# Kernel optimization log

Hardware: AMD Instinct MI355X
Metric: run time of the kernel (lower is better)

Reference implementation:

```python
import jax, jax.numpy as jnp
import numpy as np
import math

B, S, D, H = 2, 2048, 1024, 16
DH = D // H
FF = 4096
EPS = 1e-5


def _xavier(k, shape):
    lim = math.sqrt(6.0 / (shape[0] + shape[1]))
    return jax.random.uniform(k, shape, jnp.float32, -lim, lim)


def setup_inputs() -> dict:
    key = jax.random.key(0)
    ks = jax.random.split(key, 8)
    return {
        "x": jax.random.normal(ks[0], (B, S, D), jnp.float32),
        "mask": jnp.ones((B, S), jnp.int32),
        "WQ": _xavier(ks[1], (D, D)), "bQ": jnp.zeros((D,), jnp.float32),
        "WK": _xavier(ks[2], (D, D)), "bK": jnp.zeros((D,), jnp.float32),
        "WV": _xavier(ks[3], (D, D)), "bV": jnp.zeros((D,), jnp.float32),
        "WY": _xavier(ks[4], (D, D)), "bY": jnp.zeros((D,), jnp.float32),
        "ln1_w": jnp.ones((D,), jnp.float32), "ln1_b": jnp.zeros((D,), jnp.float32),
        "ln2_w": jnp.ones((D,), jnp.float32), "ln2_b": jnp.zeros((D,), jnp.float32),
        "W1": _xavier(ks[5], (D, FF)), "b1": jnp.zeros((FF,), jnp.float32),
        "W2": _xavier(ks[6], (FF, D)), "b2": jnp.zeros((D,), jnp.float32),
    }


def _layer_norm(x, w, b):
    # manual LayerNorm: biased variance over last dim
    m = jnp.mean(x, axis=-1, keepdims=True)
    v = jnp.mean(jnp.square(x - m), axis=-1, keepdims=True)
    return (x - m) / jnp.sqrt(v + EPS) * w + b


def _attention(x, mask, WQ, bQ, WK, bK, WV, bV, WY, bY):
    b, s, _ = x.shape
    def split(t):  # (B,S,D) -> (B,H,S,DH)
        return t.reshape(b, s, H, DH).transpose(0, 2, 1, 3)
    q = split(x @ WQ + bQ)
    k = split(x @ WK + bK)
    v = split(x @ WV + bV)
    scores = jnp.einsum('bhqd,bhkd->bhqk', q, k) / math.sqrt(DH)
    scores = jnp.where(mask[:, None, None, :] == 0, -jnp.inf, scores)
    w = jax.nn.softmax(scores, axis=-1)
    y = jnp.einsum('bhqk,bhkd->bhqd', w, v)
    y = y.transpose(0, 2, 1, 3).reshape(b, s, D)  # merge heads
    return y @ WY + bY


def reference(x, mask, WQ, bQ, WK, bK, WV, bV, WY, bY,
              ln1_w, ln1_b, ln2_w, ln2_b, W1, b1, W2, b2):
    a = _attention(x, mask, WQ, bQ, WK, bK, WV, bV, WY, bY)
    h = _layer_norm(a + x, ln1_w, ln1_b)
    ff = jax.nn.gelu(h @ W1 + b1, approximate=False) @ W2 + b2
    return _layer_norm(ff + h, ln2_w, ln2_b)
```

## Files before the change

### kernel.cpp

```cpp
#include <hip/hip_runtime.h>
#include <cstdint>
#include <cstddef>

#define B_ 2
#define S_ 2048
#define D_ 1024
#define H_ 16
#define DH_ 64
#define FF_ 4096
#define M_ (B_*S_)
#define MB_ ((size_t)1 << 20)
#define NT_ (S_/64)

using u16 = unsigned short;
using short8 = __attribute__((ext_vector_type(8))) short;
using short4v = __attribute__((ext_vector_type(4))) short;
using floatx4 = __attribute__((ext_vector_type(4))) float;

__device__ __forceinline__ float bf2f(u16 u) {
    return __uint_as_float(((uint32_t)u) << 16);
}
__device__ __forceinline__ u16 f2bf(float f) {
    uint32_t u = __float_as_uint(f);
    u += 0x7fffu + ((u >> 16) & 1u);
    return (u16)(u >> 16);
}
__device__ __forceinline__ uint32_t cvtpk_bf16(float lo, float hi) {
    uint32_t r;
    asm("v_cvt_pk_bf16_f32 %0, %1, %2" : "=v"(r) : "v"(lo), "v"(hi));
    return r;
}
__device__ __forceinline__ void async_copy16(const u16* g, u16* l) {
    __builtin_amdgcn_global_load_lds(
        (const __attribute__((address_space(1))) uint32_t*)g,
        (__attribute__((address_space(3))) uint32_t*)l, 16, 0, 0);
}

__global__ __launch_bounds__(256) void cvt_f32_bf16(
    const float* __restrict__ in, u16* __restrict__ out, int n)
{
    const int i = (blockIdx.x * 256 + threadIdx.x) * 4;
    if (i < n) {
        const float4 v = *(const float4*)(in + i);
        out[i + 0] = f2bf(v.x);
        out[i + 1] = f2bf(v.y);
        out[i + 2] = f2bf(v.z);
        out[i + 3] = f2bf(v.w);
    }
}

__global__ __launch_bounds__(256) void mask_bias(
    const int* __restrict__ mask, float* __restrict__ bias, int n)
{
    const int i = blockIdx.x * 256 + threadIdx.x;
    if (i < n) bias[i] = mask[i] ? 0.f : -1e30f;
}

__global__ void transpose_cvt(const float* __restrict__ in, u16* __restrict__ out,
                              int R, int C) {
    __shared__ float t[32][33];
    const int bx = blockIdx.x * 32, by = blockIdx.y * 32;
    const int tx = threadIdx.x, ty = threadIdx.y;
#pragma unroll
    for (int i = 0; i < 32; i += 8)
        t[ty + i][tx] = in[(size_t)(by + ty + i) * C + bx + tx];
    __syncthreads();
#pragma unroll
    for (int i = 0; i < 32; i += 8)
        out[(size_t)(bx + ty + i) * R + by + tx] = f2bf(t[tx][ty + i]);
}

__global__ void transpose_cvt4(
    const float* __restrict__ WQ, const float* __restrict__ WK,
    const float* __restrict__ WV, const float* __restrict__ WY,
    u16* __restrict__ Wqkvt, u16* __restrict__ WYt)
{
    __shared__ float t[32][33];
    const int zz = blockIdx.z;
    const float* in = zz == 0 ? WQ : zz == 1 ? WK : zz == 2 ? WV : WY;
    u16* out = zz < 3 ? Wqkvt + (size_t)zz * D_ * D_ : WYt;
    const int bx = blockIdx.x * 32, by = blockIdx.y * 32;
    const int tx = threadIdx.x, ty = threadIdx.y;
#pragma unroll
    for (int i = 0; i < 32; i += 8)
        t[ty + i][tx] = in[(size_t)(by + ty + i) * D_ + bx + tx];
    __syncthreads();
#pragma unroll
    for (int i = 0; i < 32; i += 8)
        out[(size_t)(bx + ty + i) * D_ + by + tx] = f2bf(t[tx][ty + i]);
}

template<bool GELU, bool OUT_F32>
__global__ __launch_bounds__(256) void gemm_bt(
    const u16* __restrict__ A, const u16* __restrict__ Bt,
    const float* __restrict__ bias, void* __restrict__ Cout,
    int M, int N, int K)
{
    __shared__ alignas(16) u16 As[128 * 32];
    __shared__ alignas(16) u16 Bs[128 * 32];
    const int tid = threadIdx.x;
    const int w = tid >> 6, lane = tid & 63;
    const int lm = lane & 15, quad = lane >> 4;
    const int wm = w >> 1, wn = w & 1;
    const size_t m0 = (size_t)blockIdx.y * 128, n0 = (size_t)blockIdx.x * 128;

    const int rowS = w * 16 + (lane >> 2);
    const int colS = (lane & 3) * 8;
    const u16* gA = A + (m0 + rowS) * K + colS;
    const u16* gB = Bt + (n0 + rowS) * K + colS;
    u16* lA = As + w * 512;
    u16* lB = Bs + w * 512;

    floatx4 acc[4][4];
    const floatx4 z = {0.f, 0.f, 0.f, 0.f};
#pragma unroll
    for (int i = 0; i < 4; ++i)
#pragma unroll
        for (int j = 0; j < 4; ++j) acc[i][j] = z;

    for (int k0 = 0; k0 < K; k0 += 32) {
        __syncthreads();
        async_copy16(gA, lA);
        async_copy16(gA + (size_t)64 * K, lA + 2048);
        async_copy16(gB, lB);
        async_copy16(gB + (size_t)64 * K, lB + 2048);
        gA += 32; gB += 32;
        __syncthreads();

        short8 af[4], bfr[4];
#pragma unroll
        for (int t = 0; t < 4; ++t)
            af[t] = *(const short8*)&As[(wm * 64 + t * 16 + lm) * 32 + quad * 8];
#pragma unroll
        for (int t = 0; t < 4; ++t)
            bfr[t] = *(const short8*)&Bs[(wn * 64 + t * 16 + lm) * 32 + quad * 8];
#pragma unroll
        for (int i = 0; i < 4; ++i)
#pragma unroll
            for (int j = 0; j < 4; ++j)
                acc[i][j] = __builtin_amdgcn_mfma_f32_16x16x32_bf16(
                    af[i], bfr[j], acc[i][j], 0, 0, 0);
    }

#pragma unroll
    for (int i = 0; i < 4; ++i) {
        const size_t r0 = m0 + wm * 64 + i * 16 + quad * 4;
#pragma unroll
        for (int j = 0; j < 4; ++j) {
            const size_t c = n0 + wn * 64 + j * 16 + lm;
            const float bv = bias[c];
#pragma unroll
            for (int t = 0; t < 4; ++t) {
                float v = acc[i][j][t] + bv;
                if (GELU) v = 0.5f * v * (1.f + erff(v * 0.70710678118f));
                if (OUT_F32) ((float*)Cout)[(r0 + t) * (size_t)N + c] = v;
                else         ((u16*)Cout)[(r0 + t) * (size_t)N + c] = f2bf(v);
            }
        }
    }
}

__global__ __launch_bounds__(256) void gemm_bt_skp(
    const u16* __restrict__ A, const u16* __restrict__ Bt,
    const float* __restrict__ bias, float* __restrict__ out0,
    float* __restrict__ Pext, int M, int N, int K)
{
    __shared__ alignas(16) u16 As[128 * 32];
    __shared__ alignas(16) u16 Bs[128 * 32];
    const int tid = threadIdx.x;
    const int w = tid >> 6, lane = tid & 63;
    const int lm = lane & 15, quad = lane >> 4;
    const int wm = w >> 1, wn = w & 1;
    const int kh = blockIdx.z;
    const int Ks = K / gridDim.z;

    const int nwg = gridDim.x * gridDim.y;
    int bid = blockIdx.y * gridDim.x + blockIdx.x;
    if ((nwg & 7) == 0) {
        const int cpx = nwg >> 3;
        bid = (bid & 7) * cpx + (bid >> 3);
    }
    const int bx = bid % gridDim.x, by = bid / gridDim.x;
    const size_t m0 = (size_t)by * 128, n0 = (size_t)bx * 128;

    const int rowS = w * 16 + (lane >> 2);
    const int colS = (lane & 3) * 8;
    const u16* gA = A + (m0 + rowS) * K + (size_t)kh * Ks + colS;
    const u16* gB = Bt + (n0 + rowS) * K + (size_t)kh * Ks + colS;
    u16* lA = As + w * 512;
    u16* lB = Bs + w * 512;

    floatx4 acc[4][4];
    const floatx4 z = {0.f, 0.f, 0.f, 0.f};
#pragma unroll
    for (int i = 0; i < 4; ++i)
#pragma unroll
        for (int j = 0; j < 4; ++j) acc[i][j] = z;

    for (int k0 = 0; k0 < Ks; k0 += 32) {
        __syncthreads();
        async_copy16(gA, lA);
        async_copy16(gA + (size_t)64 * K, lA + 2048);
        async_copy16(gB, lB);
        async_copy16(gB + (size_t)64 * K, lB + 2048);
        gA += 32; gB += 32;
        __syncthreads();

        short8 af[4], bfr[4];
#pragma unroll
        for (int t = 0; t < 4; ++t)
            af[t] = *(const short8*)&As[(wm * 64 + t * 16 + lm) * 32 + quad * 8];
#pragma unroll
        for (int t = 0; t < 4; ++t)
            bfr[t] = *(const short8*)&Bs[(wn * 64 + t * 16 + lm) * 32 + quad * 8];
#pragma unroll
        for (int i = 0; i < 4; ++i)
#pragma unroll
            for (int j = 0; j < 4; ++j)
                acc[i][j] = __builtin_amdgcn_mfma_f32_16x16x32_bf16(
                    af[i], bfr[j], acc[i][j], 0, 0, 0);
    }

    float* Cout = (kh == 0) ? out0 : Pext + (size_t)(kh - 1) * ((size_t)M * N);
#pragma unroll
    for (int i = 0; i < 4; ++i) {
        const size_t r0 = m0 + wm * 64 + i * 16 + quad * 4;
#pragma unroll
        for (int j = 0; j < 4; ++j) {
            const size_t c = n0 + wn * 64 + j * 16 + lm;
            const float bv = (kh == 0) ? bias[c] : 0.f;
#pragma unroll
            for (int t = 0; t < 4; ++t)
                Cout[(r0 + t) * (size_t)N + c] = acc[i][j][t] + bv;
        }
    }
}

__global__ __launch_bounds__(256) void gemm_bt_sk2(
    const u16* __restrict__ A, const u16* __restrict__ Bt,
    const float* __restrict__ bias, float* __restrict__ Cout,
    int M, int N, int K)
{
    __shared__ alignas(16) u16 As[128 * 32];
    __shared__ alignas(16) u16 Bs[128 * 32];
    const int tid = threadIdx.x;
    const int w = tid >> 6, lane = tid & 63;
    const int lm = lane & 15, quad = lane >> 4;
    const int wm = w >> 1, wn = w & 1;
    const int kh = blockIdx.z;
    const int Ks = K >> 1;
    const size_t m0 = (size_t)blockIdx.y * 128, n0 = (size_t)blockIdx.x * 128;

    const int rowS = w * 16 + (lane >> 2);
    const int colS = (lane & 3) * 8;
    const u16* gA = A + (m0 + rowS) * K + (size_t)kh * Ks + colS;
    const u16* gB = Bt + (n0 + rowS) * K + (size_t)kh * Ks + colS;
    u16* lA = As + w * 512;
    u16* lB = Bs + w * 512;

    floatx4 acc[4][4];
    const floatx4 z = {0.f, 0.f, 0.f, 0.f};
#pragma unroll
    for (int i = 0; i < 4; ++i)
#pragma unroll
        for (int j = 0; j < 4; ++j) acc[i][j] = z;

    for (int k0 = 0; k0 < Ks; k0 += 32) {
        __syncthreads();
        async_copy16(gA, lA);
        async_copy16(gA + (size_t)64 * K, lA + 2048);
        async_copy16(gB, lB);
        async_copy16(gB + (size_t)64 * K, lB + 2048);
        gA += 32; gB += 32;
        __syncthreads();

        short8 af[4], bfr[4];
#pragma unroll
        for (int t = 0; t < 4; ++t)
            af[t] = *(const short8*)&As[(wm * 64 + t * 16 + lm) * 32 + quad * 8];
#pragma unroll
        for (int t = 0; t < 4; ++t)
            bfr[t] = *(const short8*)&Bs[(wn * 64 + t * 16 + lm) * 32 + quad * 8];
#pragma unroll
        for (int i = 0; i < 4; ++i)
#pragma unroll
            for (int j = 0; j < 4; ++j)
                acc[i][j] = __builtin_amdgcn_mfma_f32_16x16x32_bf16(
                    af[i], bfr[j], acc[i][j], 0, 0, 0);
    }

#pragma unroll
    for (int i = 0; i < 4; ++i) {
        const size_t r0 = m0 + wm * 64 + i * 16 + quad * 4;
#pragma unroll
        for (int j = 0; j < 4; ++j) {
            const size_t c = n0 + wn * 64 + j * 16 + lm;
            const float bv = (kh == 0) ? bias[c] : 0.f;
#pragma unroll
            for (int t = 0; t < 4; ++t)
                atomicAdd(&Cout[(r0 + t) * (size_t)N + c], acc[i][j][t] + bv);
        }
    }
}

__global__ __launch_bounds__(256) void gemm_qkv(
    const u16* __restrict__ A, const u16* __restrict__ Bt,
    const float* __restrict__ bQ, const float* __restrict__ bK,
    const float* __restrict__ bV,
    u16* __restrict__ Qb, u16* __restrict__ Kb, u16* __restrict__ Vt)
{
    const int K = D_, N = 3 * D_;
    __shared__ alignas(16) u16 As[128 * 32];
    __shared__ alignas(16) u16 Bs[128 * 32];
    const int tid = threadIdx.x;
    const int w = tid >> 6, lane = tid & 63;
    const int lm = lane & 15, quad = lane >> 4;
    const int wm = w >> 1, wn = w & 1;
    const size_t m0 = (size_t)blockIdx.y * 128, n0 = (size_t)blockIdx.x * 128;

    const int rowS = w * 16 + (lane >> 2);
    const int colS = (lane & 3) * 8;
    const u16* gA = A + (m0 + rowS) * K + colS;
    const u16* gB = Bt + (n0 + rowS) * K + colS;
    u16* lA = As + w * 512;
    u16* lB = Bs + w * 512;

    floatx4 acc[4][4];
    const floatx4 z = {0.f, 0.f, 0.f, 0.f};
#pragma unroll
    for (int i = 0; i < 4; ++i)
#pragma unroll
        for (int j = 0; j < 4; ++j) acc[i][j] = z;

    for (int k0 = 0; k0 < K; k0 += 32) {
        __syncthreads();
        async_copy16(gA, lA);
        async_copy16(gA + (size_t)64 * K, lA + 2048);
        async_copy16(gB, lB);
        async_copy16(gB + (size_t)64 * K, lB + 2048);
        gA += 32; gB += 32;
        __syncthreads();

        short8 af[4], bfr[4];
#pragma unroll
        for (int t = 0; t < 4; ++t)
            af[t] = *(const short8*)&As[(wm * 64 + t * 16 + lm) * 32 + quad * 8];
#pragma unroll
        for (int t = 0; t < 4; ++t)
            bfr[t] = *(const short8*)&Bs[(wn * 64 + t * 16 + lm) * 32 + quad * 8];
#pragma unroll
        for (int i = 0; i < 4; ++i)
#pragma unroll
            for (int j = 0; j < 4; ++j)
                acc[i][j] = __builtin_amdgcn_mfma_f32_16x16x32_bf16(
                    af[i], bfr[j], acc[i][j], 0, 0, 0);
    }

#pragma unroll
    for (int i = 0; i < 4; ++i) {
        const size_t r0 = m0 + wm * 64 + i * 16 + quad * 4;
#pragma unroll
        for (int j = 0; j < 4; ++j) {
            const size_t c = n0 + wn * 64 + j * 16 + lm;
            const int sel = (int)(c >> 10);
            const int col = (int)(c & 1023);
            const float bv = sel == 0 ? bQ[col] : (sel == 1 ? bK[col] : bV[col]);
#pragma unroll
            for (int t = 0; t < 4; ++t) {
                const size_t r = r0 + t;
                const u16 v = f2bf(acc[i][j][t] + bv);
                if (sel == 0)      Qb[r * (size_t)D_ + col] = v;
                else if (sel == 1) Kb[r * (size_t)D_ + col] = v;
                else {
                    const int h = col >> 6, dh = col & 63;
                    const int bb = (int)(r >> 11), s = (int)(r & 2047);
                    Vt[((size_t)((bb * 16 + h) * 64 + dh)) * S_ + s] = v;
                }
            }
        }
    }
}

__global__ __launch_bounds__(256) void attn_kernel(
    const u16* __restrict__ Q, const u16* __restrict__ Kg,
    const u16* __restrict__ Vt, const float* __restrict__ mbias,
    u16* __restrict__ O)
{
    __shared__ alignas(16) u16 Kt[2][64 * 72];
    __shared__ alignas(16) u16 Vs[2][64 * 72];
    const int tid = threadIdx.x, w = tid >> 6, lane = tid & 63;
    const int lm = lane & 15, quad = lane >> 4;
    const int b = blockIdx.y >> 4, h = blockIdx.y & 15;
    const int q0 = blockIdx.x * 64;

    const u16* qp = Q + ((size_t)(b * S_ + q0 + w * 16 + lm)) * D_ + h * 64;
    const short8 bq0 = *(const short8*)(qp + quad * 8);
    const short8 bq1 = *(const short8*)(qp + 32 + quad * 8);

    const int sRow = tid >> 2, sCol = (tid & 3) * 16;
    const u16* gK = Kg + ((size_t)(b * S_ + sRow)) * D_ + h * 64 + sCol;
    const u16* gV = Vt + ((size_t)((b * 16 + h) * 64 + sRow)) * S_ + sCol;

    float mrow = -1e30f, lrow = 0.f;
    floatx4 o[4];
    const floatx4 z = {0.f, 0.f, 0.f, 0.f};
#pragma unroll
    for (int i = 0; i < 4; ++i) o[i] = z;

    const float* bp = mbias + b * S_;
    const float SCL = 0.18033688011112042f;

    short8 rk0 = *(const short8*)(gK);
    short8 rk1 = *(const short8*)(gK + 8);
    short8 rv0 = *(const short8*)(gV);
    short8 rv1 = *(const short8*)(gV + 8);

    for (int it = 0; it < NT_; ++it) {
        u16* kb = Kt[it & 1];
        u16* vb = Vs[it & 1];
        *(short8*)&kb[sRow * 72 + sCol]     = rk0;
        *(short8*)&kb[sRow * 72 + sCol + 8] = rk1;
        *(short8*)&vb[sRow * 72 + sCol]     = rv0;
        *(short8*)&vb[sRow * 72 + sCol + 8] = rv1;
        __syncthreads();
        if (it + 1 < NT_) {
            gK += (size_t)64 * D_; gV += 64;
            rk0 = *(const short8*)(gK);
            rk1 = *(const short8*)(gK + 8);
            rv0 = *(const short8*)(gV);
            rv1 = *(const short8*)(gV + 8);
        }

        floatx4 st[4];
        __builtin_amdgcn_s_setprio(1);
#pragma unroll
        for (int ks = 0; ks < 4; ++ks) {
            floatx4 s = z;
            const short8 ak0 = *(const short8*)&kb[(ks * 16 + lm) * 72 + quad * 8];
            const short8 ak1 = *(const short8*)&kb[(ks * 16 + lm) * 72 + 32 + quad * 8];
            s = __builtin_amdgcn_mfma_f32_16x16x32_bf16(ak0, bq0, s, 0, 0, 0);
            s = __builtin_amdgcn_mfma_f32_16x16x32_bf16(ak1, bq1, s, 0, 0, 0);
            const float4 mb4 = *(const float4*)&bp[it * 64 + ks * 16 + quad * 4];
            st[ks][0] = fmaf(s[0], SCL, mb4.x);
            st[ks][1] = fmaf(s[1], SCL, mb4.y);
            st[ks][2] = fmaf(s[2], SCL, mb4.z);
            st[ks][3] = fmaf(s[3], SCL, mb4.w);
        }
        __builtin_amdgcn_s_setprio(0);

        float t0 = fmaxf(fmaxf(st[0][0], st[0][1]), st[0][2]);
        float t1 = fmaxf(fmaxf(st[0][3], st[1][0]), st[1][1]);
        float t2 = fmaxf(fmaxf(st[1][2], st[1][3]), st[2][0]);
        float t3 = fmaxf(fmaxf(st[2][1], st[2][2]), st[2][3]);
        float t4 = fmaxf(fmaxf(st[3][0], st[3][1]), st[3][2]);
        float tm = fmaxf(fmaxf(t0, t1), t2);
        tm = fmaxf(fmaxf(tm, t3), t4);
        tm = fmaxf(tm, st[3][3]);
        tm = fmaxf(tm, __shfl_xor(tm, 16));
        tm = fmaxf(tm, __shfl_xor(tm, 32));

        if (!__all(tm <= mrow + 8.f)) {
            const float mn = fmaxf(mrow, tm);
            const float al = __builtin_amdgcn_exp2f(mrow - mn);
            mrow = mn;
            lrow *= al;
#pragma unroll
            for (int d = 0; d < 4; ++d) o[d] *= al;
        }

        float rs = 0.f;
#pragma unroll
        for (int ks = 0; ks < 4; ++ks)
#pragma unroll
            for (int r = 0; r < 4; ++r) {
                const float p = __builtin_amdgcn_exp2f(st[ks][r] - mrow);
                st[ks][r] = p; rs += p;
            }
        rs += __shfl_xor(rs, 16);
        rs += __shfl_xor(rs, 32);
        lrow += rs;

        short4v pb[4];
#pragma unroll
        for (int ks = 0; ks < 4; ++ks) {
            uint2 uu;
            uu.x = cvtpk_bf16(st[ks][0], st[ks][1]);
            uu.y = cvtpk_bf16(st[ks][2], st[ks][3]);
            pb[ks] = __builtin_bit_cast(short4v, uu);
        }
        __builtin_amdgcn_s_setprio(1);
#pragma unroll
        for (int d = 0; d < 4; ++d)
#pragma unroll
            for (int ks = 0; ks < 4; ++ks) {
                const short4v av = *(const short4v*)&vb[(d * 16 + lm) * 72 + ks * 16 + quad * 4];
                o[d] = __builtin_amdgcn_mfma_f32_16x16x16bf16_1k(av, pb[ks], o[d], 0, 0, 0);
            }
        __builtin_amdgcn_s_setprio(0);
    }
    const float inv = __builtin_amdgcn_rcpf(lrow);
    u16* op = O + ((size_t)(b * S_ + q0 + w * 16 + lm)) * D_ + h * 64 + quad * 4;
#pragma unroll
    for (int d = 0; d < 4; ++d) {
        uint2 uu;
        uu.x = cvtpk_bf16(o[d][0] * inv, o[d][1] * inv);
        uu.y = cvtpk_bf16(o[d][2] * inv, o[d][3] * inv);
        *(uint2*)(op + d * 16) = uu;
    }
}

template<bool MAIN_F32, bool RESID_F32, bool OUT_F32>
__global__ __launch_bounds__(256) void add_ln(
    const void* __restrict__ mainp, const void* __restrict__ resid,
    const float* __restrict__ gamma, const float* __restrict__ beta,
    void* __restrict__ out)
{
    const int row = blockIdx.x;
    const size_t base = (size_t)row * D_;
    const int t = threadIdx.x;
    const int w = t >> 6, lane = t & 63;
    float v[4];
#pragma unroll
    for (int i = 0; i < 4; ++i) {
        const int c = i * 256 + t;
        const float mv = MAIN_F32 ? ((const float*)mainp)[base + c]
                                  : bf2f(((const u16*)mainp)[base + c]);
        const float rv = RESID_F32 ? ((const float*)resid)[base + c]
                                   : bf2f(((const u16*)resid)[base + c]);
        v[i] = mv + rv;
    }
    float s = v[0] + v[1] + v[2] + v[3];
#pragma unroll
    for (int off = 32; off >= 1; off >>= 1) s += __shfl_xor(s, off);
    __shared__ float red[8];
    if (lane == 0) red[w] = s;
    __syncthreads();
    const float mean = (red[0] + red[1] + red[2] + red[3]) * (1.0f / D_);
    float q = 0.f;
#pragma unroll
    for (int i = 0; i < 4; ++i) { const float dd = v[i] - mean; q += dd * dd; }
#pragma unroll
    for (int off = 32; off >= 1; off >>= 1) q += __shfl_xor(q, off);
    if (lane == 0) red[4 + w] = q;
    __syncthreads();
    const float var = (red[4] + red[5] + red[6] + red[7]) * (1.0f / D_);
    const float rstd = rsqrtf(var + 1e-5f);
#pragma unroll
    for (int i = 0; i < 4; ++i) {
        const int c = i * 256 + t;
        const float o = (v[i] - mean) * rstd * gamma[c] + beta[c];
        if (OUT_F32) ((float*)out)[base + c] = o;
        else         ((u16*)out)[base + c] = f2bf(o);
    }
}

template<int NEXT, bool RESID_F32, bool OUT_F32>
__global__ __launch_bounds__(256) void add_ln_red(
    const float* __restrict__ mainp, const float* __restrict__ Pext,
    const void* __restrict__ resid,
    const float* __restrict__ gamma, const float* __restrict__ beta,
    void* __restrict__ out)
{
    const int row = blockIdx.x;
    const size_t base = (size_t)row * D_;
    const int t = threadIdx.x;
    const int w = t >> 6, lane = t & 63;
    float v[4];
#pragma unroll
    for (int i = 0; i < 4; ++i) {
        const int c = i * 256 + t;
        float s = mainp[base + c];
#pragma unroll
        for (int p = 0; p < NEXT; ++p)
            s += Pext[(size_t)p * ((size_t)M_ * D_) + base + c];
        s += RESID_F32 ? ((const float*)resid)[base + c]
                       : bf2f(((const u16*)resid)[base + c]);
        v[i] = s;
    }
    float s = v[0] + v[1] + v[2] + v[3];
#pragma unroll
    for (int off = 32; off >= 1; off >>= 1) s += __shfl_xor(s, off);
    __shared__ float red[8];
    if (lane == 0) red[w] = s;
    __syncthreads();
    const float mean = (red[0] + red[1] + red[2] + red[3]) * (1.0f / D_);
    float q = 0.f;
#pragma unroll
    for (int i = 0; i < 4; ++i) { const float dd = v[i] - mean; q += dd * dd; }
#pragma unroll
    for (int off = 32; off >= 1; off >>= 1) q += __shfl_xor(q, off);
    if (lane == 0) red[4 + w] = q;
    __syncthreads();
    const float var = (red[4] + red[5] + red[6] + red[7]) * (1.0f / D_);
    const float rstd = rsqrtf(var + 1e-5f);
#pragma unroll
    for (int i = 0; i < 4; ++i) {
        const int c = i * 256 + t;
        const float o = (v[i] - mean) * rstd * gamma[c] + beta[c];
        if (OUT_F32) ((float*)out)[base + c] = o;
        else         ((u16*)out)[base + c] = f2bf(o);
    }
}

extern "C" void kernel_launch(void* const* d_in, const int* in_sizes, int n_in,
                              void* d_out, int out_size, void* d_ws, size_t ws_size,
                              hipStream_t stream)
{
    const float* x   = (const float*)d_in[0];
    const int* mask  = (const int*)d_in[1];
    const float* WQ = (const float*)d_in[2];  const float* bQ = (const float*)d_in[3];
    const float* WK = (const float*)d_in[4];  const float* bK = (const float*)d_in[5];
    const float* WV = (const float*)d_in[6];  const float* bV = (const float*)d_in[7];
    const float* WY = (const float*)d_in[8];  const float* bY = (const float*)d_in[9];
    const float* ln1w = (const float*)d_in[10]; const float* ln1b = (const float*)d_in[11];
    const float* ln2w = (const float*)d_in[12]; const float* ln2b = (const float*)d_in[13];
    const float* W1 = (const float*)d_in[14]; const float* b1 = (const float*)d_in[15];
    const float* W2 = (const float*)d_in[16]; const float* b2 = (const float*)d_in[17];

    char* ws = (char*)d_ws;
    u16* xb    = (u16*)(ws + 0  * MB_);
    u16* Wqkvt = (u16*)(ws + 8  * MB_);
    u16* WYt   = (u16*)(ws + 14 * MB_);
    u16* Qb    = (u16*)(ws + 16 * MB_);
    u16* Kb    = (u16*)(ws + 24 * MB_);
    u16* Vt    = (u16*)(ws + 32 * MB_);
    u16* Yat   = (u16*)(ws + 40 * MB_);
    float* Ypf = (float*)(ws + 16 * MB_);
    u16* hbf   = (u16*)(ws + 8  * MB_);
    u16* W1t   = (u16*)(ws + 0  * MB_);
    u16* G     = (u16*)(ws + 16 * MB_);
    u16* W2t   = (u16*)(ws + 0  * MB_);
    float* mb  = (float*)(ws + 48 * MB_);
    float* Pext = (float*)(ws + 49 * MB_);

    const size_t PART = (size_t)M_ * D_ * sizeof(float);
    const bool ws1 = ws_size >= 49 * MB_ + 1 * PART;
    const bool ws3 = ws_size >= 49 * MB_ + 3 * PART;

    const dim3 tb(32, 8);

    cvt_f32_bf16<<<(M_*D_)/1024, 256, 0, stream>>>(x, xb, M_*D_);
    mask_bias<<<(B_*S_)/256, 256, 0, stream>>>(mask, mb, B_*S_);
    transpose_cvt4<<<dim3(D_/32, D_/32, 4), tb, 0, stream>>>(WQ, WK, WV, WY, Wqkvt, WYt);

    gemm_qkv<<<dim3(3*D_/128, M_/128), 256, 0, stream>>>(xb, Wqkvt, bQ, bK, bV, Qb, Kb, Vt);

    attn_kernel<<<dim3(S_/64, B_*H_), 256, 0, stream>>>(Qb, Kb, Vt, mb, Yat);

    if (ws1) {
        gemm_bt_skp<<<dim3(D_/128, M_/128, 2), 256, 0, stream>>>(
            Yat, WYt, bY, Ypf, Pext, M_, D_, D_);
        add_ln_red<1,true,false><<<M_, 256, 0, stream>>>(Ypf, Pext, x, ln1w, ln1b, hbf);
    } else {
        hipMemsetAsync(Ypf, 0, PART, stream);
        gemm_bt_sk2<<<dim3(D_/128, M_/128, 2), 256, 0, stream>>>(
            Yat, WYt, bY, Ypf, M_, D_, D_);
        add_ln<true,true,false><<<M_, 256, 0, stream>>>(Ypf, x, ln1w, ln1b, hbf);
    }

    transpose_cvt<<<dim3(FF_/32, D_/32), tb, 0, stream>>>(W1, W1t, D_, FF_);
    gemm_bt<true,false><<<dim3(FF_/128, M_/128), 256, 0, stream>>>(hbf, W1t, b1, G, M_, FF_, D_);

    transpose_cvt<<<dim3(D_/32, FF_/32), tb, 0, stream>>>(W2, W2t, FF_, D_);

    if (ws3) {
        gemm_bt_skp<<<dim3(D_/128, M_/128, 4), 256, 0, stream>>>(
            G, W2t, b2, (float*)d_out, Pext, M_, D_, FF_);
        add_ln_red<3,false,true><<<M_, 256, 0, stream>>>(
            (float*)d_out, Pext, hbf, ln2w, ln2b, d_out);
    } else if (ws1) {
        gemm_bt_skp<<<dim3(D_/128, M_/128, 2), 256, 0, stream>>>(
            G, W2t, b2, (float*)d_out, Pext, M_, D_, FF_);
        add_ln_red<1,false,true><<<M_, 256, 0, stream>>>(
            (float*)d_out, Pext, hbf, ln2w, ln2b, d_out);
    } else {
        hipMemsetAsync(d_out, 0, (size_t)M_ * D_ * 4, stream);
        gemm_bt_sk2<<<dim3(D_/128, M_/128, 2), 256, 0, stream>>>(
            G, W2t, b2, (float*)d_out, M_, D_, FF_);
        add_ln<true,false,true><<<M_, 256, 0, stream>>>(
            (float*)d_out, hbf, ln2w, ln2b, d_out);
    }
}
```

Baseline: 458.5 us.

## Double-buffer LDS tiles in all GEMM kernels and swizzle block order

Each GEMM kernel now keeps two LDS stages for the A and B tiles. It issues the async global-to-LDS copy for the next K step before running the MFMAs on the current stage, with one barrier per step instead of two. gemm_bt and gemm_qkv also gain the block-index remap already used by the split-K kernel, grouping workgroups to improve L2 locality. LDS use per block doubles, which may lower occupancy, and correctness depends on the async copies finishing by the end-of-step barrier.

```diff
diff --git a/kernel.cpp b/kernel.cpp
--- a/kernel.cpp
+++ b/kernel.cpp
@@ -36,6 +36,34 @@
         (__attribute__((address_space(3))) uint32_t*)l, 16, 0, 0);
 }
 
+__device__ __forceinline__ void gemm_step(
+    const u16* Acur, const u16* Bcur, u16* Astg, u16* Bstg, bool pref,
+    const u16*& gA, const u16*& gB, int K,
+    int w, int wm, int wn, int lm, int quad, floatx4 (&acc)[4][4])
+{
+    if (pref) {
+        async_copy16(gA, Astg + w * 512);
+        async_copy16(gA + (size_t)64 * K, Astg + w * 512 + 2048);
+        async_copy16(gB, Bstg + w * 512);
+        async_copy16(gB + (size_t)64 * K, Bstg + w * 512 + 2048);
+        gA += 32; gB += 32;
+    }
+    short8 af[4], bfr[4];
+#pragma unroll
+    for (int t4 = 0; t4 < 4; ++t4)
+        af[t4] = *(const short8*)&Acur[(wm * 64 + t4 * 16 + lm) * 32 + quad * 8];
+#pragma unroll
+    for (int t4 = 0; t4 < 4; ++t4)
+        bfr[t4] = *(const short8*)&Bcur[(wn * 64 + t4 * 16 + lm) * 32 + quad * 8];
+#pragma unroll
+    for (int i = 0; i < 4; ++i)
+#pragma unroll
+        for (int j = 0; j < 4; ++j)
+            acc[i][j] = __builtin_amdgcn_mfma_f32_16x16x32_bf16(
+                af[i], bfr[j], acc[i][j], 0, 0, 0);
+    __syncthreads();
+}
+
 __global__ __launch_bounds__(256) void cvt_f32_bf16(
     const float* __restrict__ in, u16* __restrict__ out, int n)
 {
@@ -96,20 +124,26 @@
     const float* __restrict__ bias, void* __restrict__ Cout,
     int M, int N, int K)
 {
-    __shared__ alignas(16) u16 As[128 * 32];
-    __shared__ alignas(16) u16 Bs[128 * 32];
+    __shared__ alignas(16) u16 As[2][128 * 32];
+    __shared__ alignas(16) u16 Bs[2][128 * 32];
     const int tid = threadIdx.x;
     const int w = tid >> 6, lane = tid & 63;
     const int lm = lane & 15, quad = lane >> 4;
     const int wm = w >> 1, wn = w & 1;
-    const size_t m0 = (size_t)blockIdx.y * 128, n0 = (size_t)blockIdx.x * 128;
+
+    const int nwg = gridDim.x * gridDim.y;
+    int bid = blockIdx.y * gridDim.x + blockIdx.x;
+    if ((nwg & 7) == 0) {
+        const int cpx = nwg >> 3;
+        bid = (bid & 7) * cpx + (bid >> 3);
+    }
+    const int bx = bid % gridDim.x, by = bid / gridDim.x;
+    const size_t m0 = (size_t)by * 128, n0 = (size_t)bx * 128;
 
     const int rowS = w * 16 + (lane >> 2);
     const int colS = (lane & 3) * 8;
     const u16* gA = A + (m0 + rowS) * K + colS;
     const u16* gB = Bt + (n0 + rowS) * K + colS;
-    u16* lA = As + w * 512;
-    u16* lB = Bs + w * 512;
 
     floatx4 acc[4][4];
     const floatx4 z = {0.f, 0.f, 0.f, 0.f};
@@ -118,28 +152,19 @@
 #pragma unroll
         for (int j = 0; j < 4; ++j) acc[i][j] = z;
 
-    for (int k0 = 0; k0 < K; k0 += 32) {
-        __syncthreads();
-        async_copy16(gA, lA);
-        async_copy16(gA + (size_t)64 * K, lA + 2048);
-        async_copy16(gB, lB);
-        async_copy16(gB + (size_t)64 * K, lB + 2048);
-        gA += 32; gB += 32;
-        __syncthreads();
-
-        short8 af[4], bfr[4];
-#pragma unroll
-        for (int t = 0; t < 4; ++t)
-            af[t] = *(const short8*)&As[(wm * 64 + t * 16 + lm) * 32 + quad * 8];
-#pragma unroll
-        for (int t = 0; t < 4; ++t)
-            bfr[t] = *(const short8*)&Bs[(wn * 64 + t * 16 + lm) * 32 + quad * 8];
-#pragma unroll
-        for (int i = 0; i < 4; ++i)
-#pragma unroll
-            for (int j = 0; j < 4; ++j)
-                acc[i][j] = __builtin_amdgcn_mfma_f32_16x16x32_bf16(
-                    af[i], bfr[j], acc[i][j], 0, 0, 0);
+    async_copy16(gA, &As[0][w * 512]);
+    async_copy16(gA + (size_t)64 * K, &As[0][w * 512 + 2048]);
+    async_copy16(gB, &Bs[0][w * 512]);
+    async_copy16(gB + (size_t)64 * K, &Bs[0][w * 512 + 2048]);
+    gA += 32; gB += 32;
+    __syncthreads();
+
+    const int nk = K >> 5;
+    for (int t = 0; t < nk; t += 2) {
+        gemm_step(As[0], Bs[0], As[1], Bs[1], true,
+                  gA, gB, K, w, wm, wn, lm, quad, acc);
+        gemm_step(As[1], Bs[1], As[0], Bs[0], t + 2 < nk,
+                  gA, gB, K, w, wm, wn, lm, quad, acc);
     }
 
 #pragma unroll
@@ -165,8 +190,8 @@
     const float* __restrict__ bias, float* __restrict__ out0,
     float* __restrict__ Pext, int M, int N, int K)
 {
-    __shared__ alignas(16) u16 As[128 * 32];
-    __shared__ alignas(16) u16 Bs[128 * 32];
+    __shared__ alignas(16) u16 As[2][128 * 32];
+    __shared__ alignas(16) u16 Bs[2][128 * 32];
     const int tid = threadIdx.x;
     const int w = tid >> 6, lane = tid & 63;
     const int lm = lane & 15, quad = lane >> 4;
@@ -187,8 +212,6 @@
     const int colS = (lane & 3) * 8;
     const u16* gA = A + (m0 + rowS) * K + (size_t)kh * Ks + colS;
     const u16* gB = Bt + (n0 + rowS) * K + (size_t)kh * Ks + colS;
-    u16* lA = As + w * 512;
-    u16* lB = Bs + w * 512;
 
     floatx4 acc[4][4];
     const floatx4 z = {0.f, 0.f, 0.f, 0.f};
@@ -197,28 +220,19 @@
 #pragma unroll
         for (int j = 0; j < 4; ++j) acc[i][j] = z;
 
-    for (int k0 = 0; k0 < Ks; k0 += 32) {
-        __syncthreads();
-        async_copy16(gA, lA);
-        async_copy16(gA + (size_t)64 * K, lA + 2048);
-        async_copy16(gB, lB);
-        async_copy16(gB + (size_t)64 * K, lB + 2048);
-        gA += 32; gB += 32;
-        __syncthreads();
-
-        short8 af[4], bfr[4];
-#pragma unroll
-        for (int t = 0; t < 4; ++t)
-            af[t] = *(const short8*)&As[(wm * 64 + t * 16 + lm) * 32 + quad * 8];
-#pragma unroll
-        for (int t = 0; t < 4; ++t)
-            bfr[t] = *(const short8*)&Bs[(wn * 64 + t * 16 + lm) * 32 + quad * 8];
-#pragma unroll
-        for (int i = 0; i < 4; ++i)
-#pragma unroll
-            for (int j = 0; j < 4; ++j)
-                acc[i][j] = __builtin_amdgcn_mfma_f32_16x16x32_bf16(
-                    af[i], bfr[j], acc[i][j], 0, 0, 0);
+    async_copy16(gA, &As[0][w * 512]);
+    async_copy16(gA + (size_t)64 * K, &As[0][w * 512 + 2048]);
+    async_copy16(gB, &Bs[0][w * 512]);
+    async_copy16(gB + (size_t)64 * K, &Bs[0][w * 512 + 2048]);
+    gA += 32; gB += 32;
+    __syncthreads();
+
+    const int nk = Ks >> 5;
+    for (int t = 0; t < nk; t += 2) {
+        gemm_step(As[0], Bs[0], As[1], Bs[1], true,
+                  gA, gB, K, w, wm, wn, lm, quad, acc);
+        gemm_step(As[1], Bs[1], As[0], Bs[0], t + 2 < nk,
+                  gA, gB, K, w, wm, wn, lm, quad, acc);
     }
 
     float* Cout = (kh == 0) ? out0 : Pext + (size_t)(kh - 1) * ((size_t)M * N);
@@ -241,8 +255,8 @@
     const float* __restrict__ bias, float* __restrict__ Cout,
     int M, int N, int K)
 {
-    __shared__ alignas(16) u16 As[128 * 32];
-    __shared__ alignas(16) u16 Bs[128 * 32];
+    __shared__ alignas(16) u16 As[2][128 * 32];
+    __shared__ alignas(16) u16 Bs[2][128 * 32];
     const int tid = threadIdx.x;
     const int w = tid >> 6, lane = tid & 63;
     const int lm = lane & 15, quad = lane >> 4;
@@ -255,8 +269,6 @@
     const int colS = (lane & 3) * 8;
     const u16* gA = A + (m0 + rowS) * K + (size_t)kh * Ks + colS;
     const u16* gB = Bt + (n0 + rowS) * K + (size_t)kh * Ks + colS;
-    u16* lA = As + w * 512;
-    u16* lB = Bs + w * 512;
 
     floatx4 acc[4][4];
     const floatx4 z = {0.f, 0.f, 0.f, 0.f};
@@ -265,28 +277,19 @@
 #pragma unroll
         for (int j = 0; j < 4; ++j) acc[i][j] = z;
 
-    for (int k0 = 0; k0 < Ks; k0 += 32) {
-        __syncthreads();
-        async_copy16(gA, lA);
-        async_copy16(gA + (size_t)64 * K, lA + 2048);
-        async_copy16(gB, lB);
-        async_copy16(gB + (size_t)64 * K, lB + 2048);
-        gA += 32; gB += 32;
-        __syncthreads();
-
-        short8 af[4], bfr[4];
-#pragma unroll
-        for (int t = 0; t < 4; ++t)
-            af[t] = *(const short8*)&As[(wm * 64 + t * 16 + lm) * 32 + quad * 8];
-#pragma unroll
-        for (int t = 0; t < 4; ++t)
-            bfr[t] = *(const short8*)&Bs[(wn * 64 + t * 16 + lm) * 32 + quad * 8];
-#pragma unroll
-        for (int i = 0; i < 4; ++i)
-#pragma unroll
-            for (int j = 0; j < 4; ++j)
-                acc[i][j] = __builtin_amdgcn_mfma_f32_16x16x32_bf16(
-                    af[i], bfr[j], acc[i][j], 0, 0, 0);
+    async_copy16(gA, &As[0][w * 512]);
+    async_copy16(gA + (size_t)64 * K, &As[0][w * 512 + 2048]);
+    async_copy16(gB, &Bs[0][w * 512]);
+    async_copy16(gB + (size_t)64 * K, &Bs[0][w * 512 + 2048]);
+    gA += 32; gB += 32;
+    __syncthreads();
+
+    const int nk = Ks >> 5;
+    for (int t = 0; t < nk; t += 2) {
+        gemm_step(As[0], Bs[0], As[1], Bs[1], true,
+                  gA, gB, K, w, wm, wn, lm, quad, acc);
+        gemm_step(As[1], Bs[1], As[0], Bs[0], t + 2 < nk,
+                  gA, gB, K, w, wm, wn, lm, quad, acc);
     }
 
 #pragma unroll
@@ -310,20 +313,26 @@
     u16* __restrict__ Qb, u16* __restrict__ Kb, u16* __restrict__ Vt)
 {
     const int K = D_, N = 3 * D_;
-    __shared__ alignas(16) u16 As[128 * 32];
-    __shared__ alignas(16) u16 Bs[128 * 32];
+    __shared__ alignas(16) u16 As[2][128 * 32];
+    __shared__ alignas(16) u16 Bs[2][128 * 32];
     const int tid = threadIdx.x;
     const int w = tid >> 6, lane = tid & 63;
     const int lm = lane & 15, quad = lane >> 4;
     const int wm = w >> 1, wn = w & 1;
-    const size_t m0 = (size_t)blockIdx.y * 128, n0 = (size_t)blockIdx.x * 128;
+
+    const int nwg = gridDim.x * gridDim.y;
+    int bid = blockIdx.y * gridDim.x + blockIdx.x;
+    if ((nwg & 7) == 0) {
+        const int cpx = nwg >> 3;
+        bid = (bid & 7) * cpx + (bid >> 3);
+    }
+    const int bx = bid % gridDim.x, by = bid / gridDim.x;
+    const size_t m0 = (size_t)by * 128, n0 = (size_t)bx * 128;
 
     const int rowS = w * 16 + (lane >> 2);
     const int colS = (lane & 3) * 8;
     const u16* gA = A + (m0 + rowS) * K + colS;
     const u16* gB = Bt + (n0 + rowS) * K + colS;
-    u16* lA = As + w * 512;
-    u16* lB = Bs + w * 512;
 
     floatx4 acc[4][4];
     const floatx4 z = {0.f, 0.f, 0.f, 0.f};
@@ -332,28 +341,19 @@
 #pragma unroll
         for (int j = 0; j < 4; ++j) acc[i][j] = z;
 
-    for (int k0 = 0; k0 < K; k0 += 32) {
-        __syncthreads();
-        async_copy16(gA, lA);
-        async_copy16(gA + (size_t)64 * K, lA + 2048);
-        async_copy16(gB, lB);
-        async_copy16(gB + (size_t)64 * K, lB + 2048);
-        gA += 32; gB += 32;
-        __syncthreads();
-
-        short8 af[4], bfr[4];
-#pragma unroll
-        for (int t = 0; t < 4; ++t)
-            af[t] = *(const short8*)&As[(wm * 64 + t * 16 + lm) * 32 + quad * 8];
-#pragma unroll
-        for (int t = 0; t < 4; ++t)
-            bfr[t] = *(const short8*)&Bs[(wn * 64 + t * 16 + lm) * 32 + quad * 8];
-#pragma unroll
-        for (int i = 0; i < 4; ++i)
-#pragma unroll
-            for (int j = 0; j < 4; ++j)
-                acc[i][j] = __builtin_amdgcn_mfma_f32_16x16x32_bf16(
-                    af[i], bfr[j], acc[i][j], 0, 0, 0);
+    async_copy16(gA, &As[0][w * 512]);
+    async_copy16(gA + (size_t)64 * K, &As[0][w * 512 + 2048]);
+    async_copy16(gB, &Bs[0][w * 512]);
+    async_copy16(gB + (size_t)64 * K, &Bs[0][w * 512 + 2048]);
+    gA += 32; gB += 32;
+    __syncthreads();
+
+    const int nk = K >> 5;
+    for (int t = 0; t < nk; t += 2) {
+        gemm_step(As[0], Bs[0], As[1], Bs[1], true,
+                  gA, gB, K, w, wm, wn, lm, quad, acc);
+        gemm_step(As[1], Bs[1], As[0], Bs[0], t + 2 < nk,
+                  gA, gB, K, w, wm, wn, lm, quad, acc);
     }
 
 #pragma unroll
```

Result: faster. 447.5 us (-2.4%).
